# Performance work log

Measured on AMD Instinct MI355X. Metric: run time of the kernel, lower is better.

The kernel has to match this reference:

```python
import jax, jax.numpy as jnp
import numpy as np

N = 100000
E = 1000000
F = 64

def setup_inputs() -> dict:
    key = jax.random.key(0)
    k1, k2, k3 = jax.random.split(key, 3)
    x = jax.random.normal(k1, (N, F), dtype=jnp.float32)
    edge_weight = jax.random.uniform(k2, (E,), dtype=jnp.float32)
    edge_index = jax.random.randint(k3, (2, E), 0, N, dtype=jnp.int64)
    return {"x": x, "edge_weight": edge_weight, "edge_index": edge_index, "num_nodes": N}

def reference(x, edge_weight, edge_index, num_nodes):
    # flow='source_to_target': j=0 (source, gathered), i=1 (target, scattered)
    src, dst = edge_index[0], edge_index[1]
    # message: gather source features, scale by edge weight -> [E, F]
    msg = edge_weight[:, None] * x[src]
    # aggregate: scatter_add into zero-initialized [num_nodes, F]
    out = jax.ops.segment_sum(msg, dst, num_segments=num_nodes)
    return out
```

## Files before the change

kernel.cpp:

```cpp
#include <hip/hip_runtime.h>


#define FDIM 64
#define BSHIFT 7
#define BNODES 128
#define BMAX 1024
#define SLOT 1536
#define SC_EPB 4096
#define SC_KPT 16
#define H_EPT 8
#define H_EPB (256 * H_EPT)
#define CAP 2048
#define A_THREADS 512
#define A_KPT (CAP / A_THREADS)

__global__ void __launch_bounds__(256)
scatter_edges_kernel(const float* __restrict__ x,
                     const float* __restrict__ w,
                     const int* __restrict__ src,
                     const int* __restrict__ dst,
                     float* __restrict__ out,
                     int E) {
    int gid = blockIdx.x * blockDim.x + threadIdx.x;
    int e = gid >> 4;
    int q = gid & 15;
    if (e >= E) return;
    int s = src[e];
    int d = dst[e];
    float we = w[e];
    const float4* xrow = reinterpret_cast<const float4*>(x + (size_t)s * FDIM);
    float4 v = xrow[q];
    float* o = out + (size_t)d * FDIM + q * 4;
    atomicAdd(o + 0, we * v.x);
    atomicAdd(o + 1, we * v.y);
    atomicAdd(o + 2, we * v.z);
    atomicAdd(o + 3, we * v.w);
}

__device__ __forceinline__ unsigned int bf16rn(float f) {
    unsigned int u = __float_as_uint(f);
    u += 0x7fffu + ((u >> 16) & 1u);
    return u >> 16;
}

__global__ void __launch_bounds__(256)
conv_bf16(const float* __restrict__ x, uint4* __restrict__ xb, int total8,
          int* __restrict__ cursor, int B, int slot) {
    int i = blockIdx.x * 256 + threadIdx.x;
    if (slot > 0 && i < B) cursor[i] = i * slot;
    if (i >= total8) return;
    const float4* p = reinterpret_cast<const float4*>(x) + (size_t)i * 2;
    float4 a = p[0], b = p[1];
    uint4 o;
    o.x = bf16rn(a.x) | (bf16rn(a.y) << 16);
    o.y = bf16rn(a.z) | (bf16rn(a.w) << 16);
    o.z = bf16rn(b.x) | (bf16rn(b.y) << 16);
    o.w = bf16rn(b.z) | (bf16rn(b.w) << 16);
    xb[i] = o;
}

__global__ void __launch_bounds__(256)
bucket_hist(const int* __restrict__ dst, int* __restrict__ bcnt, int E, int B) {
    __shared__ int h[BMAX];
    int t = threadIdx.x;
    for (int i = t; i < B; i += 256) h[i] = 0;
    __syncthreads();
    int base = blockIdx.x * H_EPB + t * H_EPT;
    if (base + H_EPT <= E) {
        int4 a = *reinterpret_cast<const int4*>(dst + base);
        int4 b = *reinterpret_cast<const int4*>(dst + base + 4);
        atomicAdd(&h[a.x >> BSHIFT], 1); atomicAdd(&h[a.y >> BSHIFT], 1);
        atomicAdd(&h[a.z >> BSHIFT], 1); atomicAdd(&h[a.w >> BSHIFT], 1);
        atomicAdd(&h[b.x >> BSHIFT], 1); atomicAdd(&h[b.y >> BSHIFT], 1);
        atomicAdd(&h[b.z >> BSHIFT], 1); atomicAdd(&h[b.w >> BSHIFT], 1);
    } else {
        for (int k = 0; k < H_EPT; ++k) {
            int e = base + k;
            if (e < E) atomicAdd(&h[dst[e] >> BSHIFT], 1);
        }
    }
    __syncthreads();
    for (int i = t; i < B; i += 256) if (h[i]) atomicAdd(&bcnt[i], h[i]);
}

__global__ void __launch_bounds__(1024)
bucket_scan(const int* __restrict__ bcnt, int* __restrict__ boff,
            int* __restrict__ cursor, int B, int E) {
    __shared__ int sh[1024];
    int t = threadIdx.x;
    int v = (t < B) ? bcnt[t] : 0;
    sh[t] = v;
    __syncthreads();
    for (int d = 1; d < 1024; d <<= 1) {
        int u = (t >= d) ? sh[t - d] : 0;
        __syncthreads();
        sh[t] += u;
        __syncthreads();
    }
    if (t < B) { int ex = sh[t] - v; boff[t] = ex; cursor[t] = ex; }
    if (t == 0) boff[B] = E;
}

__global__ void __launch_bounds__(256)
bucket_scatter(const int* __restrict__ src, const int* __restrict__ dst,
               const float* __restrict__ w, int* __restrict__ cursor,
               int2* __restrict__ rec, int E, int B, int slot) {
    __shared__ int2 lrec[SC_EPB];
    __shared__ unsigned short lbin[SC_EPB];
    __shared__ int h[BMAX];
    __shared__ int noff[BMAX];
    __shared__ int cbase[BMAX];
    __shared__ int part[256];
    int t = threadIdx.x;
    for (int i = t; i < B; i += 256) h[i] = 0;
    __syncthreads();

    int blk = blockIdx.x * SC_EPB;
    int cnt = E - blk; if (cnt > SC_EPB) cnt = SC_EPB;

    int sv[SC_KPT]; int dv[SC_KPT]; float wv[SC_KPT];
    int bkt[SC_KPT]; int rnk[SC_KPT]; int pv[SC_KPT];
    int base = blk + t * SC_KPT;
    if (base + SC_KPT <= E) {
        #pragma unroll
        for (int k = 0; k < SC_KPT / 4; ++k) {
            *reinterpret_cast<int4*>(sv + k * 4) =
                *reinterpret_cast<const int4*>(src + base + k * 4);
            *reinterpret_cast<int4*>(dv + k * 4) =
                *reinterpret_cast<const int4*>(dst + base + k * 4);
            *reinterpret_cast<float4*>(wv + k * 4) =
                *reinterpret_cast<const float4*>(w + base + k * 4);
        }
        #pragma unroll
        for (int k = 0; k < SC_KPT; ++k) {
            int bb = dv[k] >> BSHIFT;
            bkt[k] = bb;
            pv[k] = sv[k] | ((dv[k] & (BNODES - 1)) << 17);
            rnk[k] = atomicAdd(&h[bb], 1);
        }
    } else {
        #pragma unroll
        for (int k = 0; k < SC_KPT; ++k) {
            int e = base + k;
            if (e < E) {
                int d = dst[e];
                int bb = d >> BSHIFT;
                bkt[k] = bb;
                pv[k] = src[e] | ((d & (BNODES - 1)) << 17);
                wv[k] = w[e];
                rnk[k] = atomicAdd(&h[bb], 1);
            } else bkt[k] = -1;
        }
    }
    __syncthreads();

    int bpt = (B + 255) >> 8;
    int s = 0;
    for (int k = 0; k < bpt; ++k) {
        int i = t * bpt + k;
        if (i < B) s += h[i];
    }
    part[t] = s;
    __syncthreads();
    for (int d = 1; d < 256; d <<= 1) {
        int u = (t >= d) ? part[t - d] : 0;
        __syncthreads();
        part[t] += u;
        __syncthreads();
    }
    int run = part[t] - s;
    for (int k = 0; k < bpt; ++k) {
        int i = t * bpt + k;
        if (i < B) { noff[i] = run; run += h[i]; }
    }
    __syncthreads();

    #pragma unroll
    for (int k = 0; k < SC_KPT; ++k) {
        if (bkt[k] >= 0) {
            int p = noff[bkt[k]] + rnk[k];
            int2 r; r.x = pv[k]; r.y = __float_as_int(wv[k]);
            lrec[p] = r;
            lbin[p] = (unsigned short)bkt[k];
        }
    }
    for (int i = t; i < B; i += 256)
        if (h[i]) cbase[i] = atomicAdd(&cursor[i], h[i]);
    __syncthreads();

    for (int i = t; i < cnt; i += 256) {
        int b = lbin[i];
        int idx = cbase[b] + (i - noff[b]);
        if (slot > 0 && idx >= (b + 1) * slot) continue;
        rec[idx] = lrec[i];
    }
}

__device__ __forceinline__ void acc8(const uint4& u, float wv,
                                     float4& a0, float4& a1) {
    a0.x += wv * __uint_as_float(u.x << 16);
    a0.y += wv * __uint_as_float(u.x & 0xFFFF0000u);
    a0.z += wv * __uint_as_float(u.y << 16);
    a0.w += wv * __uint_as_float(u.y & 0xFFFF0000u);
    a1.x += wv * __uint_as_float(u.z << 16);
    a1.y += wv * __uint_as_float(u.z & 0xFFFF0000u);
    a1.z += wv * __uint_as_float(u.w << 16);
    a1.w += wv * __uint_as_float(u.w & 0xFFFF0000u);
}

__global__ void __launch_bounds__(A_THREADS)
bucket_sort_accum(const uint4* __restrict__ xb, const int2* __restrict__ rec,
                  const int* __restrict__ boff, const int* __restrict__ cursor,
                  int slot, float* __restrict__ out, int N) {
    __shared__ int2 lrec[CAP];
    __shared__ int nhist[BNODES];
    __shared__ int sscan[BNODES];
    __shared__ int noff[BNODES];
    int b = blockIdx.x;
    int t = threadIdx.x;
    int g = t >> 3;
    int q = t & 7;
    int beg, end;
    if (slot > 0) {
        beg = b * slot;
        int c = cursor[b] - beg; if (c > slot) c = slot;
        end = beg + c;
    } else {
        beg = boff[b]; end = boff[b + 1];
    }

    float4 acc[2][2];
    #pragma unroll
    for (int j = 0; j < 2; ++j) {
        acc[j][0] = make_float4(0.f, 0.f, 0.f, 0.f);
        acc[j][1] = make_float4(0.f, 0.f, 0.f, 0.f);
    }

    for (int pos = beg; pos < end; pos += CAP) {
        int cnt = end - pos; if (cnt > CAP) cnt = CAP;
        if (t < BNODES) nhist[t] = 0;
        __syncthreads();
        int2 myrec[A_KPT]; int myrank[A_KPT]; int mybin[A_KPT];
        #pragma unroll
        for (int k = 0; k < A_KPT; ++k) {
            int i = k * A_THREADS + t;
            if (i < cnt) {
                int2 r = rec[pos + i];
                int bin = (r.x >> 17) & (BNODES - 1);
                myrec[k] = r;
                mybin[k] = bin;
                myrank[k] = atomicAdd(&nhist[bin], 1);
            } else mybin[k] = -1;
        }
        __syncthreads();
        int v = (t < BNODES) ? nhist[t] : 0;
        if (t < BNODES) sscan[t] = v;
        __syncthreads();
        #pragma unroll
        for (int d = 1; d < BNODES; d <<= 1) {
            int u = (t >= d && t < BNODES) ? sscan[t - d] : 0;
            __syncthreads();
            if (t < BNODES) sscan[t] += u;
            __syncthreads();
        }
        if (t < BNODES) noff[t] = sscan[t] - v;
        __syncthreads();
        #pragma unroll
        for (int k = 0; k < A_KPT; ++k)
            if (mybin[k] >= 0) lrec[noff[mybin[k]] + myrank[k]] = myrec[k];
        __syncthreads();

        #pragma unroll
        for (int j = 0; j < 2; ++j) {
            int n = j * 64 + g;
            int sb = noff[n];
            int se = sb + nhist[n];
            int i = sb;
            for (; i + 4 <= se; i += 4) {
                int2 r0 = lrec[i + 0], r1 = lrec[i + 1];
                int2 r2 = lrec[i + 2], r3 = lrec[i + 3];
                uint4 u0 = xb[(size_t)(r0.x & 0x1FFFF) * 8 + q];
                uint4 u1 = xb[(size_t)(r1.x & 0x1FFFF) * 8 + q];
                uint4 u2 = xb[(size_t)(r2.x & 0x1FFFF) * 8 + q];
                uint4 u3 = xb[(size_t)(r3.x & 0x1FFFF) * 8 + q];
                acc8(u0, __int_as_float(r0.y), acc[j][0], acc[j][1]);
                acc8(u1, __int_as_float(r1.y), acc[j][0], acc[j][1]);
                acc8(u2, __int_as_float(r2.y), acc[j][0], acc[j][1]);
                acc8(u3, __int_as_float(r3.y), acc[j][0], acc[j][1]);
            }
            for (; i < se; ++i) {
                int2 r = lrec[i];
                uint4 u = xb[(size_t)(r.x & 0x1FFFF) * 8 + q];
                acc8(u, __int_as_float(r.y), acc[j][0], acc[j][1]);
            }
        }
        __syncthreads();
    }

    int nodeBase = b << BSHIFT;
    #pragma unroll
    for (int j = 0; j < 2; ++j) {
        int row = nodeBase + j * 64 + g;
        if (row < N) {
            float4* o = reinterpret_cast<float4*>(out + ((size_t)row << 6)) + q * 2;
            o[0] = acc[j][0];
            o[1] = acc[j][1];
        }
    }
}

extern "C" void kernel_launch(void* const* d_in, const int* in_sizes, int n_in,
                              void* d_out, int out_size, void* d_ws, size_t ws_size,
                              hipStream_t stream) {
    const float* x  = (const float*)d_in[0];
    const float* w  = (const float*)d_in[1];
    const int* eidx = (const int*)d_in[2];
    int E = in_sizes[1];
    int N = out_size / FDIM;
    const int* src = eidx;
    const int* dst = eidx + E;
    float* out = (float*)d_out;

    int B = (N + BNODES - 1) >> BSHIFT;
    int total8 = N * (FDIM / 8);
    int gridC = (total8 + 255) / 256;
    int gridS = (E + SC_EPB - 1) / SC_EPB;
    size_t xb_bytes = (size_t)N * FDIM * sizeof(unsigned short);

    if (B <= BMAX && N <= (1 << 17)) {
        {
            int* cursor = (int*)d_ws;
            size_t rec_off = ((size_t)B * sizeof(int) + 15) & ~(size_t)15;
            int2* rec = (int2*)((char*)d_ws + rec_off);
            size_t xb_off = (rec_off + (size_t)B * SLOT * sizeof(int2) + 15) & ~(size_t)15;
            uint4* xb = (uint4*)((char*)d_ws + xb_off);
            size_t need = xb_off + xb_bytes;
            if (ws_size >= need) {
                conv_bf16<<<gridC, 256, 0, stream>>>(x, xb, total8, cursor, B, SLOT);
                bucket_scatter<<<gridS, 256, 0, stream>>>(src, dst, w, cursor, rec, E, B, SLOT);
                bucket_sort_accum<<<B, A_THREADS, 0, stream>>>(xb, rec, (const int*)nullptr,
                                                               cursor, SLOT, out, N);
                return;
            }
        }
        {
            int* bcnt   = (int*)d_ws;
            int* boff   = bcnt + B;
            int* cursor = boff + B + 1;
            size_t rec_off = (((size_t)(3 * B + 1)) * sizeof(int) + 15) & ~(size_t)15;
            int2* rec = (int2*)((char*)d_ws + rec_off);
            size_t xb_off = (rec_off + (size_t)E * sizeof(int2) + 15) & ~(size_t)15;
            uint4* xb = (uint4*)((char*)d_ws + xb_off);
            size_t need = xb_off + xb_bytes;
            if (ws_size >= need) {
                hipMemsetAsync(bcnt, 0, (size_t)B * sizeof(int), stream);
                conv_bf16<<<gridC, 256, 0, stream>>>(x, xb, total8, cursor, B, 0);
                int gridH = (E + H_EPB - 1) / H_EPB;
                bucket_hist<<<gridH, 256, 0, stream>>>(dst, bcnt, E, B);
                bucket_scan<<<1, 1024, 0, stream>>>(bcnt, boff, cursor, B, E);
                bucket_scatter<<<gridS, 256, 0, stream>>>(src, dst, w, cursor, rec, E, B, 0);
                bucket_sort_accum<<<B, A_THREADS, 0, stream>>>(xb, rec, boff,
                                                               cursor, 0, out, N);
                return;
            }
        }
    }

    hipMemsetAsync(out, 0, (size_t)out_size * sizeof(float), stream);
    int grid = (E * 16 + 255) / 256;
    scatter_edges_kernel<<<grid, 256, 0, stream>>>(x, w, src, dst, out, E);
}
```

Before: 137.3 us.

## Widen scatter and accumulate kernels to 1024 threads with fewer items per thread

The bucket scatter kernel now runs 1024 threads per block over 2048 edges, so each thread handles 2 edges instead of 16, and the launch grid doubles. The accumulate kernel uses 1024 threads so each 8-lane group owns one destination node instead of two, and its staging capacity grows to 4096 records. The aim is more parallelism and memory-level concurrency per block and less per-thread serial gather work. In exchange, the block-level scans are longer, there is more scatter-block overhead, and larger blocks may reduce occupancy.

```diff
diff --git a/kernel.cpp b/kernel.cpp
--- a/kernel.cpp
+++ b/kernel.cpp
@@ -6,12 +6,13 @@
 #define BNODES 128
 #define BMAX 1024
 #define SLOT 1536
-#define SC_EPB 4096
-#define SC_KPT 16
+#define SC_EPB 2048
+#define SC_THREADS 1024
+#define SC_KPT (SC_EPB / SC_THREADS)
 #define H_EPT 8
 #define H_EPB (256 * H_EPT)
-#define CAP 2048
-#define A_THREADS 512
+#define CAP 4096
+#define A_THREADS 1024
 #define A_KPT (CAP / A_THREADS)
 
 __global__ void __launch_bounds__(256)
@@ -101,7 +102,7 @@
     if (t == 0) boff[B] = E;
 }
 
-__global__ void __launch_bounds__(256)
+__global__ void __launch_bounds__(SC_THREADS)
 bucket_scatter(const int* __restrict__ src, const int* __restrict__ dst,
                const float* __restrict__ w, int* __restrict__ cursor,
                int2* __restrict__ rec, int E, int B, int slot) {
@@ -110,27 +111,23 @@
     __shared__ int h[BMAX];
     __shared__ int noff[BMAX];
     __shared__ int cbase[BMAX];
-    __shared__ int part[256];
+    __shared__ int part[SC_THREADS];
     int t = threadIdx.x;
-    for (int i = t; i < B; i += 256) h[i] = 0;
+    for (int i = t; i < B; i += SC_THREADS) h[i] = 0;
     __syncthreads();
 
     int blk = blockIdx.x * SC_EPB;
     int cnt = E - blk; if (cnt > SC_EPB) cnt = SC_EPB;
 
-    int sv[SC_KPT]; int dv[SC_KPT]; float wv[SC_KPT];
-    int bkt[SC_KPT]; int rnk[SC_KPT]; int pv[SC_KPT];
+    int bkt[SC_KPT]; int rnk[SC_KPT]; int pv[SC_KPT]; float wv[SC_KPT];
     int base = blk + t * SC_KPT;
     if (base + SC_KPT <= E) {
-        #pragma unroll
-        for (int k = 0; k < SC_KPT / 4; ++k) {
-            *reinterpret_cast<int4*>(sv + k * 4) =
-                *reinterpret_cast<const int4*>(src + base + k * 4);
-            *reinterpret_cast<int4*>(dv + k * 4) =
-                *reinterpret_cast<const int4*>(dst + base + k * 4);
-            *reinterpret_cast<float4*>(wv + k * 4) =
-                *reinterpret_cast<const float4*>(w + base + k * 4);
-        }
+        int2 s2 = *reinterpret_cast<const int2*>(src + base);
+        int2 d2 = *reinterpret_cast<const int2*>(dst + base);
+        float2 w2 = *reinterpret_cast<const float2*>(w + base);
+        int sv[SC_KPT] = { s2.x, s2.y };
+        int dv[SC_KPT] = { d2.x, d2.y };
+        wv[0] = w2.x; wv[1] = w2.y;
         #pragma unroll
         for (int k = 0; k < SC_KPT; ++k) {
             int bb = dv[k] >> BSHIFT;
@@ -154,7 +151,7 @@
     }
     __syncthreads();
 
-    int bpt = (B + 255) >> 8;
+    int bpt = (B + SC_THREADS - 1) / SC_THREADS;
     int s = 0;
     for (int k = 0; k < bpt; ++k) {
         int i = t * bpt + k;
@@ -162,7 +159,7 @@
     }
     part[t] = s;
     __syncthreads();
-    for (int d = 1; d < 256; d <<= 1) {
+    for (int d = 1; d < SC_THREADS; d <<= 1) {
         int u = (t >= d) ? part[t - d] : 0;
         __syncthreads();
         part[t] += u;
@@ -184,11 +181,11 @@
             lbin[p] = (unsigned short)bkt[k];
         }
     }
-    for (int i = t; i < B; i += 256)
+    for (int i = t; i < B; i += SC_THREADS)
         if (h[i]) cbase[i] = atomicAdd(&cursor[i], h[i]);
     __syncthreads();
 
-    for (int i = t; i < cnt; i += 256) {
+    for (int i = t; i < cnt; i += SC_THREADS) {
         int b = lbin[i];
         int idx = cbase[b] + (i - noff[b]);
         if (slot > 0 && idx >= (b + 1) * slot) continue;
@@ -229,12 +226,8 @@
         beg = boff[b]; end = boff[b + 1];
     }
 
-    float4 acc[2][2];
-    #pragma unroll
-    for (int j = 0; j < 2; ++j) {
-        acc[j][0] = make_float4(0.f, 0.f, 0.f, 0.f);
-        acc[j][1] = make_float4(0.f, 0.f, 0.f, 0.f);
-    }
+    float4 acc0 = make_float4(0.f, 0.f, 0.f, 0.f);
+    float4 acc1 = make_float4(0.f, 0.f, 0.f, 0.f);
 
     for (int pos = beg; pos < end; pos += CAP) {
         int cnt = end - pos; if (cnt > CAP) cnt = CAP;
@@ -270,11 +263,9 @@
             if (mybin[k] >= 0) lrec[noff[mybin[k]] + myrank[k]] = myrec[k];
         __syncthreads();
 
-        #pragma unroll
-        for (int j = 0; j < 2; ++j) {
-            int n = j * 64 + g;
-            int sb = noff[n];
-            int se = sb + nhist[n];
+        {
+            int sb = noff[g];
+            int se = sb + nhist[g];
             int i = sb;
             for (; i + 4 <= se; i += 4) {
                 int2 r0 = lrec[i + 0], r1 = lrec[i + 1];
@@ -283,29 +274,25 @@
                 uint4 u1 = xb[(size_t)(r1.x & 0x1FFFF) * 8 + q];
                 uint4 u2 = xb[(size_t)(r2.x & 0x1FFFF) * 8 + q];
                 uint4 u3 = xb[(size_t)(r3.x & 0x1FFFF) * 8 + q];
-                acc8(u0, __int_as_float(r0.y), acc[j][0], acc[j][1]);
-                acc8(u1, __int_as_float(r1.y), acc[j][0], acc[j][1]);
-                acc8(u2, __int_as_float(r2.y), acc[j][0], acc[j][1]);
-                acc8(u3, __int_as_float(r3.y), acc[j][0], acc[j][1]);
+                acc8(u0, __int_as_float(r0.y), acc0, acc1);
+                acc8(u1, __int_as_float(r1.y), acc0, acc1);
+                acc8(u2, __int_as_float(r2.y), acc0, acc1);
+                acc8(u3, __int_as_float(r3.y), acc0, acc1);
             }
             for (; i < se; ++i) {
                 int2 r = lrec[i];
                 uint4 u = xb[(size_t)(r.x & 0x1FFFF) * 8 + q];
-                acc8(u, __int_as_float(r.y), acc[j][0], acc[j][1]);
+                acc8(u, __int_as_float(r.y), acc0, acc1);
             }
         }
         __syncthreads();
     }
 
-    int nodeBase = b << BSHIFT;
-    #pragma unroll
-    for (int j = 0; j < 2; ++j) {
-        int row = nodeBase + j * 64 + g;
-        if (row < N) {
-            float4* o = reinterpret_cast<float4*>(out + ((size_t)row << 6)) + q * 2;
-            o[0] = acc[j][0];
-            o[1] = acc[j][1];
-        }
+    int row = (b << BSHIFT) + g;
+    if (row < N) {
+        float4* o = reinterpret_cast<float4*>(out + ((size_t)row << 6)) + q * 2;
+        o[0] = acc0;
+        o[1] = acc1;
     }
 }
 
@@ -337,7 +324,7 @@
             size_t need = xb_off + xb_bytes;
             if (ws_size >= need) {
                 conv_bf16<<<gridC, 256, 0, stream>>>(x, xb, total8, cursor, B, SLOT);
-                bucket_scatter<<<gridS, 256, 0, stream>>>(src, dst, w, cursor, rec, E, B, SLOT);
+                bucket_scatter<<<gridS, SC_THREADS, 0, stream>>>(src, dst, w, cursor, rec, E, B, SLOT);
                 bucket_sort_accum<<<B, A_THREADS, 0, stream>>>(xb, rec, (const int*)nullptr,
                                                                cursor, SLOT, out, N);
                 return;
@@ -358,7 +345,7 @@
                 int gridH = (E + H_EPB - 1) / H_EPB;
                 bucket_hist<<<gridH, 256, 0, stream>>>(dst, bcnt, E, B);
                 bucket_scan<<<1, 1024, 0, stream>>>(bcnt, boff, cursor, B, E);
-                bucket_scatter<<<gridS, 256, 0, stream>>>(src, dst, w, cursor, rec, E, B, 0);
+                bucket_scatter<<<gridS, SC_THREADS, 0, stream>>>(src, dst, w, cursor, rec, E, B, 0);
                 bucket_sort_accum<<<B, A_THREADS, 0, stream>>>(xb, rec, boff,
                                                                cursor, 0, out, N);
                 return;
```

Result: slower. 148.5 us (+8.2%).

## Use wavefront shuffle scans and smaller, wider scatter blocks

Applied to the files above, without the earlier changes.

Replaces the shared-memory Hillis-Steele prefix scans in bucket_scatter and bucket_sort_accum with wavefront __shfl_up scans plus a small cross-wave combine. This removes many __syncthreads barriers per block. The scatter kernel now handles 2048 edges per block with 512 threads (4 per thread instead of 16), which gives more blocks and less register pressure. Launch bounds now request higher occupancy. Side effects are more global cursor atomics per edge and a hard-coded hv[2] array that assumes B <= 1024.

```diff
diff --git a/kernel.cpp b/kernel.cpp
--- a/kernel.cpp
+++ b/kernel.cpp
@@ -6,8 +6,9 @@
 #define BNODES 128
 #define BMAX 1024
 #define SLOT 1536
-#define SC_EPB 4096
-#define SC_KPT 16
+#define SC_EPB 2048
+#define SC_THREADS 512
+#define SC_KPT (SC_EPB / SC_THREADS)
 #define H_EPT 8
 #define H_EPB (256 * H_EPT)
 #define CAP 2048
@@ -101,7 +102,7 @@
     if (t == 0) boff[B] = E;
 }
 
-__global__ void __launch_bounds__(256)
+__global__ void __launch_bounds__(SC_THREADS, 8)
 bucket_scatter(const int* __restrict__ src, const int* __restrict__ dst,
                const float* __restrict__ w, int* __restrict__ cursor,
                int2* __restrict__ rec, int E, int B, int slot) {
@@ -110,27 +111,26 @@
     __shared__ int h[BMAX];
     __shared__ int noff[BMAX];
     __shared__ int cbase[BMAX];
-    __shared__ int part[256];
+    __shared__ int wsum[SC_THREADS / 64];
+    __shared__ int wexc[SC_THREADS / 64];
     int t = threadIdx.x;
-    for (int i = t; i < B; i += 256) h[i] = 0;
+    int lane = t & 63;
+    int wid = t >> 6;
+    for (int i = t; i < B; i += SC_THREADS) h[i] = 0;
     __syncthreads();
 
     int blk = blockIdx.x * SC_EPB;
     int cnt = E - blk; if (cnt > SC_EPB) cnt = SC_EPB;
 
-    int sv[SC_KPT]; int dv[SC_KPT]; float wv[SC_KPT];
-    int bkt[SC_KPT]; int rnk[SC_KPT]; int pv[SC_KPT];
+    int bkt[SC_KPT]; int rnk[SC_KPT]; int pv[SC_KPT]; float wv[SC_KPT];
     int base = blk + t * SC_KPT;
     if (base + SC_KPT <= E) {
-        #pragma unroll
-        for (int k = 0; k < SC_KPT / 4; ++k) {
-            *reinterpret_cast<int4*>(sv + k * 4) =
-                *reinterpret_cast<const int4*>(src + base + k * 4);
-            *reinterpret_cast<int4*>(dv + k * 4) =
-                *reinterpret_cast<const int4*>(dst + base + k * 4);
-            *reinterpret_cast<float4*>(wv + k * 4) =
-                *reinterpret_cast<const float4*>(w + base + k * 4);
-        }
+        int4 s4 = *reinterpret_cast<const int4*>(src + base);
+        int4 d4 = *reinterpret_cast<const int4*>(dst + base);
+        float4 w4 = *reinterpret_cast<const float4*>(w + base);
+        int sv[SC_KPT] = { s4.x, s4.y, s4.z, s4.w };
+        int dv[SC_KPT] = { d4.x, d4.y, d4.z, d4.w };
+        wv[0] = w4.x; wv[1] = w4.y; wv[2] = w4.z; wv[3] = w4.w;
         #pragma unroll
         for (int k = 0; k < SC_KPT; ++k) {
             int bb = dv[k] >> BSHIFT;
@@ -154,24 +154,37 @@
     }
     __syncthreads();
 
-    int bpt = (B + 255) >> 8;
+    int bpt = (B + SC_THREADS - 1) / SC_THREADS;
+    int hv[2] = {0, 0};
     int s = 0;
+    int i0 = t * bpt;
     for (int k = 0; k < bpt; ++k) {
-        int i = t * bpt + k;
-        if (i < B) s += h[i];
-    }
-    part[t] = s;
-    __syncthreads();
-    for (int d = 1; d < 256; d <<= 1) {
-        int u = (t >= d) ? part[t - d] : 0;
-        __syncthreads();
-        part[t] += u;
-        __syncthreads();
-    }
-    int run = part[t] - s;
+        int i = i0 + k;
+        if (i < B) { hv[k] = h[i]; s += hv[k]; }
+    }
+    int v = s;
+    #pragma unroll
+    for (int d = 1; d < 64; d <<= 1) {
+        int u = __shfl_up(v, d);
+        if (lane >= d) v += u;
+    }
+    if (lane == 63) wsum[wid] = v;
+    __syncthreads();
+    if (wid == 0 && lane < SC_THREADS / 64) {
+        int wv2 = wsum[lane];
+        int vv = wv2;
+        #pragma unroll
+        for (int d = 1; d < SC_THREADS / 64; d <<= 1) {
+            int u = __shfl_up(vv, d, SC_THREADS / 64);
+            if (lane >= d) vv += u;
+        }
+        wexc[lane] = vv - wv2;
+    }
+    __syncthreads();
+    int run = wexc[wid] + (v - s);
     for (int k = 0; k < bpt; ++k) {
-        int i = t * bpt + k;
-        if (i < B) { noff[i] = run; run += h[i]; }
+        int i = i0 + k;
+        if (i < B) { noff[i] = run; run += hv[k]; }
     }
     __syncthreads();
 
@@ -184,11 +197,11 @@
             lbin[p] = (unsigned short)bkt[k];
         }
     }
-    for (int i = t; i < B; i += 256)
+    for (int i = t; i < B; i += SC_THREADS)
         if (h[i]) cbase[i] = atomicAdd(&cursor[i], h[i]);
     __syncthreads();
 
-    for (int i = t; i < cnt; i += 256) {
+    for (int i = t; i < cnt; i += SC_THREADS) {
         int b = lbin[i];
         int idx = cbase[b] + (i - noff[b]);
         if (slot > 0 && idx >= (b + 1) * slot) continue;
@@ -208,14 +221,14 @@
     a1.w += wv * __uint_as_float(u.w & 0xFFFF0000u);
 }
 
-__global__ void __launch_bounds__(A_THREADS)
+__global__ void __launch_bounds__(A_THREADS, 8)
 bucket_sort_accum(const uint4* __restrict__ xb, const int2* __restrict__ rec,
                   const int* __restrict__ boff, const int* __restrict__ cursor,
                   int slot, float* __restrict__ out, int N) {
     __shared__ int2 lrec[CAP];
     __shared__ int nhist[BNODES];
-    __shared__ int sscan[BNODES];
     __shared__ int noff[BNODES];
+    __shared__ int swtot;
     int b = blockIdx.x;
     int t = threadIdx.x;
     int g = t >> 3;
@@ -223,7 +236,9 @@
     int beg, end;
     if (slot > 0) {
         beg = b * slot;
-        int c = cursor[b] - beg; if (c > slot) c = slot;
+        int c = cursor[b] - beg;
+        if (c > slot) c = slot;
+        if (c < 0) c = 0;
         end = beg + c;
     } else {
         beg = boff[b]; end = boff[b + 1];
@@ -253,17 +268,20 @@
             } else mybin[k] = -1;
         }
         __syncthreads();
-        int v = (t < BNODES) ? nhist[t] : 0;
-        if (t < BNODES) sscan[t] = v;
-        __syncthreads();
-        #pragma unroll
-        for (int d = 1; d < BNODES; d <<= 1) {
-            int u = (t >= d && t < BNODES) ? sscan[t - d] : 0;
-            __syncthreads();
-            if (t < BNODES) sscan[t] += u;
-            __syncthreads();
-        }
-        if (t < BNODES) noff[t] = sscan[t] - v;
+        int hv = 0, v = 0;
+        if (t < BNODES) {
+            hv = nhist[t];
+            v = hv;
+            #pragma unroll
+            for (int d = 1; d < 64; d <<= 1) {
+                int u = __shfl_up(v, d);
+                if ((t & 63) >= d) v += u;
+            }
+        }
+        if (t == 63) swtot = v;
+        __syncthreads();
+        if (t >= 64 && t < BNODES) v += swtot;
+        if (t < BNODES) noff[t] = v - hv;
         __syncthreads();
         #pragma unroll
         for (int k = 0; k < A_KPT; ++k)
@@ -337,7 +355,7 @@
             size_t need = xb_off + xb_bytes;
             if (ws_size >= need) {
                 conv_bf16<<<gridC, 256, 0, stream>>>(x, xb, total8, cursor, B, SLOT);
-                bucket_scatter<<<gridS, 256, 0, stream>>>(src, dst, w, cursor, rec, E, B, SLOT);
+                bucket_scatter<<<gridS, SC_THREADS, 0, stream>>>(src, dst, w, cursor, rec, E, B, SLOT);
                 bucket_sort_accum<<<B, A_THREADS, 0, stream>>>(xb, rec, (const int*)nullptr,
                                                                cursor, SLOT, out, N);
                 return;
@@ -358,7 +376,7 @@
                 int gridH = (E + H_EPB - 1) / H_EPB;
                 bucket_hist<<<gridH, 256, 0, stream>>>(dst, bcnt, E, B);
                 bucket_scan<<<1, 1024, 0, stream>>>(bcnt, boff, cursor, B, E);
-                bucket_scatter<<<gridS, 256, 0, stream>>>(src, dst, w, cursor, rec, E, B, 0);
+                bucket_scatter<<<gridS, SC_THREADS, 0, stream>>>(src, dst, w, cursor, rec, E, B, 0);
                 bucket_sort_accum<<<B, A_THREADS, 0, stream>>>(xb, rec, boff,
                                                                cursor, 0, out, N);
                 return;
```

Result: slower. 152.3 us (+10.9%).
